# Kernel tuning notes

Hardware: AMD Instinct MI355X
Metric: run time of the kernel (lower is better)

## Reference

```python
import jax, jax.numpy as jnp
import numpy as np

N_PAD = 2097152   # padded node count at this depth (H)
N_KEPT = 1048576  # non-empty node count after depad
C = 32            # feature channels


def setup_inputs() -> dict:
    key = jax.random.key(0)
    data_in = jax.random.normal(key, (1, C, N_PAD, 1), dtype=jnp.float32)
    # kept_idx: sorted unique indices of non-empty octree nodes (children >= 0)
    rng = np.random.default_rng(0)
    kept = np.sort(rng.choice(N_PAD, size=N_KEPT, replace=False)).astype(np.int64)
    kept_idx = jnp.asarray(kept)
    return {"data_in": data_in, "kept_idx": kept_idx}


def reference(data_in, kept_idx):
    # octree_depad: compact node features by gathering non-empty nodes.
    # data_in: [1, C, N_PAD, 1] -> data_out: [1, C, N_KEPT, 1]
    return jnp.take(data_in, kept_idx, axis=2)
```

## Files before the change

kernel.cpp:

```cpp
#include <hip/hip_runtime.h>

#define NCH 32

__global__ __launch_bounds__(256) void octree_depad_kernel(
    const float* __restrict__ in,
    const int* __restrict__ idx,
    float* __restrict__ out,
    int n_kept, int n_pad) {
    int k4 = blockIdx.x * blockDim.x + threadIdx.x;
    int total4 = n_kept >> 2;

    if (k4 < total4) {
        int k = k4 << 2;
        int4 iv = *reinterpret_cast<const int4*>(idx + k);
        long long i0 = iv.x, i1 = iv.y, i2 = iv.z, i3 = iv.w;

        #pragma unroll 8
        for (int c = 0; c < NCH; ++c) {
            const float* src = in + (size_t)c * (size_t)n_pad;
            float4 v;
            v.x = src[i0];
            v.y = src[i1];
            v.z = src[i2];
            v.w = src[i3];
            *reinterpret_cast<float4*>(out + (size_t)c * (size_t)n_kept + k) = v;
        }
    }

    int tail_start = total4 << 2;
    int n_tail = n_kept - tail_start;
    if (n_tail > 0 && blockIdx.x == 0 && (int)threadIdx.x < n_tail) {
        int k = tail_start + threadIdx.x;
        long long s = idx[k];
        #pragma unroll 8
        for (int c = 0; c < NCH; ++c) {
            out[(size_t)c * (size_t)n_kept + k] = in[(size_t)c * (size_t)n_pad + s];
        }
    }
}

extern "C" void kernel_launch(void* const* d_in, const int* in_sizes, int n_in,
                              void* d_out, int out_size, void* d_ws, size_t ws_size,
                              hipStream_t stream) {
    const float* in  = (const float*)d_in[0];
    const int*   idx = (const int*)d_in[1];
    float*       out = (float*)d_out;

    int n_kept = in_sizes[1];
    int n_pad  = in_sizes[0] / NCH;

    int total4 = (n_kept + 3) >> 2;
    int block  = 256;
    int grid   = (total4 + block - 1) / block;

    octree_depad_kernel<<<grid, block, 0, stream>>>(in, idx, out, n_kept, n_pad);
}
```

Before: 401.0 us.

## Stage contiguous input span in LDS per tile before scattering gathered outputs

Each block handles 1024 kept indices, computes the contiguous source span they cover, and for every channel loads that span into shared memory with coalesced float4 reads before gathering from LDS. This replaces scattered global 4-byte reads with streaming loads. The cost is a pair of barriers per channel, scalar rather than vectorized output stores, and a fallback to direct gathers when the span exceeds the LDS buffer.

```diff
diff --git a/kernel.cpp b/kernel.cpp
--- a/kernel.cpp
+++ b/kernel.cpp
@@ -1,40 +1,64 @@
 #include <hip/hip_runtime.h>
 
 #define NCH 32
+#define BLOCK 256
+#define K_TILE 1024
+#define PER_T (K_TILE / BLOCK)
+#define LDS_FLOATS 3072
 
-__global__ __launch_bounds__(256) void octree_depad_kernel(
+__global__ __launch_bounds__(BLOCK) void octree_depad_lds(
     const float* __restrict__ in,
     const int* __restrict__ idx,
     float* __restrict__ out,
     int n_kept, int n_pad) {
-    int k4 = blockIdx.x * blockDim.x + threadIdx.x;
-    int total4 = n_kept >> 2;
+    __shared__ float lds[LDS_FLOATS];
 
-    if (k4 < total4) {
-        int k = k4 << 2;
-        int4 iv = *reinterpret_cast<const int4*>(idx + k);
-        long long i0 = iv.x, i1 = iv.y, i2 = iv.z, i3 = iv.w;
+    const int t  = threadIdx.x;
+    const int k0 = blockIdx.x * K_TILE;
+    const int kend  = min(k0 + K_TILE, n_kept);
+    const int klast = kend - 1;
 
-        #pragma unroll 8
-        for (int c = 0; c < NCH; ++c) {
-            const float* src = in + (size_t)c * (size_t)n_pad;
-            float4 v;
-            v.x = src[i0];
-            v.y = src[i1];
-            v.z = src[i2];
-            v.w = src[i3];
-            *reinterpret_cast<float4*>(out + (size_t)c * (size_t)n_kept + k) = v;
-        }
+    const int first = idx[k0];
+    const int last  = idx[klast];
+    const int base  = first & ~3;
+    const int span  = last - base + 1;
+
+    int  kk[PER_T];
+    int  loc[PER_T];
+    bool valid[PER_T];
+#pragma unroll
+    for (int j = 0; j < PER_T; ++j) {
+        int k = k0 + j * BLOCK + t;
+        kk[j] = k;
+        valid[j] = (k < kend);
+        loc[j] = valid[j] ? (idx[k] - base) : 0;
     }
 
-    int tail_start = total4 << 2;
-    int n_tail = n_kept - tail_start;
-    if (n_tail > 0 && blockIdx.x == 0 && (int)threadIdx.x < n_tail) {
-        int k = tail_start + threadIdx.x;
-        long long s = idx[k];
-        #pragma unroll 8
+    if (span <= LDS_FLOATS) {
+        int nf4 = (span + 3) >> 2;
+        int maxf4 = (n_pad - base) >> 2;
+        if (nf4 > maxf4) nf4 = maxf4;
+
         for (int c = 0; c < NCH; ++c) {
-            out[(size_t)c * (size_t)n_kept + k] = in[(size_t)c * (size_t)n_pad + s];
+            const float4* src =
+                reinterpret_cast<const float4*>(in + (size_t)c * n_pad + base);
+            __syncthreads();
+            for (int i = t; i < nf4; i += BLOCK)
+                reinterpret_cast<float4*>(lds)[i] = src[i];
+            __syncthreads();
+
+            float* dst = out + (size_t)c * n_kept;
+#pragma unroll
+            for (int j = 0; j < PER_T; ++j)
+                if (valid[j]) dst[kk[j]] = lds[loc[j]];
+        }
+    } else {
+        for (int c = 0; c < NCH; ++c) {
+            const float* src = in + (size_t)c * n_pad;
+            float* dst = out + (size_t)c * n_kept;
+#pragma unroll
+            for (int j = 0; j < PER_T; ++j)
+                if (valid[j]) dst[kk[j]] = src[(size_t)base + loc[j]];
         }
     }
 }
@@ -49,9 +73,6 @@
     int n_kept = in_sizes[1];
     int n_pad  = in_sizes[0] / NCH;
 
-    int total4 = (n_kept + 3) >> 2;
-    int block  = 256;
-    int grid   = (total4 + block - 1) / block;
-
-    octree_depad_kernel<<<grid, block, 0, stream>>>(in, idx, out, n_kept, n_pad);
+    int grid = (n_kept + K_TILE - 1) / K_TILE;
+    octree_depad_lds<<<grid, BLOCK, 0, stream>>>(in, idx, out, n_kept, n_pad);
 }
```

After: 400.3 us. Within noise of the previous version (-0.2%).

## Stage contiguous input span per wave in LDS before gathering

Applied to the files above, without the earlier changes.

Each wave handles 256 sorted kept indices and copies the contiguous input window they cover (up to 768 floats per channel) into LDS with coalesced float4 loads. It then gathers from LDS instead of issuing scattered global loads. This is meant to replace scattered 4-byte global reads with dense vector reads, since roughly half the nodes are kept. The cost is extra LDS traffic, a double-buffered LDS array, a fallback path for wide spans, and reliance on the per-wave wavefront executing in lockstep without explicit barriers.

```diff
diff --git a/kernel.cpp b/kernel.cpp
--- a/kernel.cpp
+++ b/kernel.cpp
@@ -1,40 +1,83 @@
 #include <hip/hip_runtime.h>
 
 #define NCH 32
+#define BLOCK 256
+#define WAVES 4
+#define PER_LANE 4
+#define WAVE_K (64 * PER_LANE)
+#define WSPAN 768
 
-__global__ __launch_bounds__(256) void octree_depad_kernel(
+__global__ __launch_bounds__(BLOCK) void octree_depad_wave(
     const float* __restrict__ in,
     const int* __restrict__ idx,
     float* __restrict__ out,
     int n_kept, int n_pad) {
-    int k4 = blockIdx.x * blockDim.x + threadIdx.x;
-    int total4 = n_kept >> 2;
+    __shared__ float lds[WAVES][2][WSPAN];
 
-    if (k4 < total4) {
-        int k = k4 << 2;
+    const int lane = threadIdx.x & 63;
+    const int wid  = threadIdx.x >> 6;
+    const int gw   = blockIdx.x * WAVES + wid;
+    const int wbase = gw * WAVE_K;
+    if (wbase >= n_kept) return;
+    const int kend  = min(wbase + WAVE_K, n_kept);
+    const int klast = kend - 1;
+
+    const int base4 = idx[wbase] & ~3;
+    const int span  = idx[klast] - base4 + 1;
+
+    const int k = wbase + lane * PER_LANE;
+    const bool any  = (k < kend);
+    const bool full = (k + PER_LANE <= kend);
+    int i0 = 0, i1 = 0, i2 = 0, i3 = 0;
+    if (full) {
         int4 iv = *reinterpret_cast<const int4*>(idx + k);
-        long long i0 = iv.x, i1 = iv.y, i2 = iv.z, i3 = iv.w;
-
-        #pragma unroll 8
-        for (int c = 0; c < NCH; ++c) {
-            const float* src = in + (size_t)c * (size_t)n_pad;
-            float4 v;
-            v.x = src[i0];
-            v.y = src[i1];
-            v.z = src[i2];
-            v.w = src[i3];
-            *reinterpret_cast<float4*>(out + (size_t)c * (size_t)n_kept + k) = v;
-        }
+        i0 = iv.x; i1 = iv.y; i2 = iv.z; i3 = iv.w;
+    } else if (any) {
+        i0 = idx[k];
+        i1 = (k + 1 < kend) ? idx[k + 1] : i0;
+        i2 = (k + 2 < kend) ? idx[k + 2] : i0;
+        i3 = (k + 3 < kend) ? idx[k + 3] : i0;
     }
 
-    int tail_start = total4 << 2;
-    int n_tail = n_kept - tail_start;
-    if (n_tail > 0 && blockIdx.x == 0 && (int)threadIdx.x < n_tail) {
-        int k = tail_start + threadIdx.x;
-        long long s = idx[k];
-        #pragma unroll 8
+    if (span <= WSPAN) {
+        int nf4 = (span + 3) >> 2;
+        const int cap = (n_pad - base4) >> 2;
+        if (nf4 > cap) nf4 = cap;
+        const int l0 = i0 - base4, l1 = i1 - base4,
+                  l2 = i2 - base4, l3 = i3 - base4;
+
         for (int c = 0; c < NCH; ++c) {
-            out[(size_t)c * (size_t)n_kept + k] = in[(size_t)c * (size_t)n_pad + s];
+            float* buf = lds[wid][c & 1];
+            const float4* src =
+                reinterpret_cast<const float4*>(in + (size_t)c * n_pad + base4);
+            for (int i = lane; i < nf4; i += 64)
+                reinterpret_cast<float4*>(buf)[i] = src[i];
+            if (any) {
+                float4 o;
+                o.x = buf[l0]; o.y = buf[l1]; o.z = buf[l2]; o.w = buf[l3];
+                float* dst = out + (size_t)c * n_kept + k;
+                if (full) {
+                    *reinterpret_cast<float4*>(dst) = o;
+                } else {
+                    dst[0] = o.x;
+                    if (k + 1 < kend) dst[1] = o.y;
+                    if (k + 2 < kend) dst[2] = o.z;
+                }
+            }
+        }
+    } else {
+        for (int c = 0; c < NCH; ++c) {
+            const float* src = in + (size_t)c * n_pad;
+            float* dst = out + (size_t)c * n_kept;
+            if (full) {
+                float4 o;
+                o.x = src[i0]; o.y = src[i1]; o.z = src[i2]; o.w = src[i3];
+                *reinterpret_cast<float4*>(dst + k) = o;
+            } else if (any) {
+                dst[k] = src[i0];
+                if (k + 1 < kend) dst[k + 1] = src[i1];
+                if (k + 2 < kend) dst[k + 2] = src[i2];
+            }
         }
     }
 }
@@ -49,9 +92,6 @@
     int n_kept = in_sizes[1];
     int n_pad  = in_sizes[0] / NCH;
 
-    int total4 = (n_kept + 3) >> 2;
-    int block  = 256;
-    int grid   = (total4 + block - 1) / block;
-
-    octree_depad_kernel<<<grid, block, 0, stream>>>(in, idx, out, n_kept, n_pad);
+    int grid = (n_kept + WAVES * WAVE_K - 1) / (WAVES * WAVE_K);
+    octree_depad_wave<<<grid, BLOCK, 0, stream>>>(in, idx, out, n_kept, n_pad);
 }
```

After: 399.8 us. About the same (-0.3%).
